# Kernel optimization log

Measured on AMD Instinct MI355X. Metric: run time of the kernel, lower is better.

## Reference

```python
import jax, jax.numpy as jnp
import numpy as np

N = 50000        # nodes
E = 800000       # edges (avg degree 16)
F_IN = 128
H = 128
C = 16


def setup_inputs() -> dict:
    key = jax.random.key(0)
    ks = jax.random.split(key, 12)
    x = jax.random.normal(ks[0], (N, F_IN), dtype=jnp.float32)
    edges = jax.random.randint(ks[1], (2, E), 0, N, dtype=jnp.int32)
    dims = [(F_IN, H), (H, H // 2), (H // 2, H // 4), (H // 4, H // 8), (H // 8, C)]
    params = {}
    for i, (di, do) in enumerate(dims):
        params[f"W{i+1}"] = jax.random.normal(ks[2 + 2 * i], (di, do), dtype=jnp.float32) * (1.0 / np.sqrt(di)).astype(np.float32)
        params[f"b{i+1}"] = jax.random.normal(ks[3 + 2 * i], (do,), dtype=jnp.float32) * 0.01
    return {"x": x, "edges": edges, **params}


def reference(x, edges, W1, b1, W2, b2, W3, b3, W4, b4, W5, b5):
    src, dst = edges[0], edges[1]
    ones = jnp.ones((E,), x.dtype)
    # symmetric ('both') normalization with degree clamped to >= 1 (DGL GraphConv default)
    out_deg = jnp.clip(jax.ops.segment_sum(ones, src, num_segments=N), 1.0, None)
    in_deg = jnp.clip(jax.ops.segment_sum(ones, dst, num_segments=N), 1.0, None)
    norm_src = (out_deg ** -0.5)[:, None]   # [N,1]
    norm_dst = (in_deg ** -0.5)[:, None]    # [N,1]

    def graph_conv(h, W, b):
        h = h @ W                                  # dense transform first (out <= in)
        msgs = (h * norm_src)[src]                 # [E, d_out] gather
        agg = jax.ops.segment_sum(msgs, dst, num_segments=N)  # scatter-add SpMM
        return agg * norm_dst + b

    h = x
    for W, b in ((W1, b1), (W2, b2), (W3, b3), (W4, b4), (W5, b5)):
        h = jax.nn.relu(graph_conv(h, W, b))
    return h
```

## Files before the change

kernel.cpp:

```cpp
#include <hip/hip_runtime.h>
#include <hip/hip_bf16.h>


#define THREADS 256
#define HIST_B 256
#define HWORDS 12500
#define RS_BLOCKS 196
#define G1BLKS 1564

typedef __attribute__((ext_vector_type(8))) short short8_t;
typedef __attribute__((ext_vector_type(4))) float float4_t;

__device__ __forceinline__ unsigned short f2bf_rne(float f) {
    unsigned u = __builtin_bit_cast(unsigned, f);
    unsigned r = u + 0x7fffu + ((u >> 16) & 1u);
    return (unsigned short)(r >> 16);
}
__device__ __forceinline__ float bf2f(unsigned short h) {
    return __builtin_bit_cast(float, ((unsigned)h) << 16);
}

template<int NT, bool NORM>
__device__ __forceinline__ void quant_epilogue(float4_t* acc, const float* __restrict__ norm,
                                               short* __restrict__ outq, float* __restrict__ qscale,
                                               int M, int blk, int tid,
                                               int ostride, int ocol0, int qstride, int qoff) {
    const int w    = tid >> 6;
    const int lane = tid & 63;
    const int ln   = lane & 15;
    const int quad = lane >> 4;
    const int orow = blk * 64 + w * 16 + quad * 4;
#pragma unroll
    for (int i = 0; i < 4; ++i) {
        int r = orow + i;
        float m = 0.f;
#pragma unroll
        for (int nt = 0; nt < NT; ++nt) m = fmaxf(m, fabsf(acc[nt][i]));
#pragma unroll
        for (int off = 1; off < 16; off <<= 1) m = fmaxf(m, __shfl_xor(m, off));
        float s = 1.f;
        if (NORM) s = (r < M) ? norm[r] : 0.f;
        float rowmax = m * s;
        float inv = (rowmax > 0.f) ? (32767.f / rowmax) : 0.f;
        if (r < M) {
            if (ln == 0) qscale[r * qstride + qoff] = rowmax * (1.f / 32767.f);
#pragma unroll
            for (int nt = 0; nt < NT; ++nt)
                outq[(size_t)r * ostride + ocol0 + nt * 16 + ln] =
                    (short)(int)__builtin_rintf(acc[nt][i] * s * inv);
        }
    }
}

template<int K, int NOUT, bool NORM>
__device__ __forceinline__ void gemm_core(const float* __restrict__ A,
                                          const short* lh, const short* ll,
                                          const float* __restrict__ norm,
                                          short* __restrict__ outq, float* __restrict__ qscale,
                                          int M, int blk, int tid,
                                          int ostride, int ocol0, int qstride, int qoff) {
    constexpr int Kp  = (K + 31) & ~31;
    constexpr int STR = Kp + 8;
    constexpr int NT  = NOUT / 16;
    const int w    = tid >> 6;
    const int lane = tid & 63;
    const int ln   = lane & 15;
    const int quad = lane >> 4;
    const int row  = blk * 64 + w * 16 + ln;
    const bool rv  = row < M;

    float4_t acc[NT];
#pragma unroll
    for (int i = 0; i < NT; ++i) acc[i] = (float4_t){0.f, 0.f, 0.f, 0.f};

#pragma unroll
    for (int kt = 0; kt < Kp / 32; ++kt) {
        const int k0 = kt * 32 + quad * 8;
        float a[8];
        if (rv && k0 < K) {
            float4 v0 = *(const float4*)&A[(size_t)row * K + k0];
            float4 v1 = *(const float4*)&A[(size_t)row * K + k0 + 4];
            a[0] = v0.x; a[1] = v0.y; a[2] = v0.z; a[3] = v0.w;
            a[4] = v1.x; a[5] = v1.y; a[6] = v1.z; a[7] = v1.w;
        } else {
#pragma unroll
            for (int j = 0; j < 8; ++j) a[j] = 0.f;
        }
        short8_t ahi, alo;
#pragma unroll
        for (int j = 0; j < 8; ++j) {
            unsigned short h = f2bf_rne(a[j]);
            ahi[j] = (short)h;
            alo[j] = (short)f2bf_rne(a[j] - bf2f(h));
        }
#pragma unroll
        for (int nt = 0; nt < NT; ++nt) {
            const int bidx = (nt * 16 + ln) * STR + kt * 32 + quad * 8;
            short8_t bh = *(const short8_t*)&lh[bidx];
            short8_t bl = *(const short8_t*)&ll[bidx];
            acc[nt] = __builtin_amdgcn_mfma_f32_16x16x32_bf16(ahi, bh, acc[nt], 0, 0, 0);
            acc[nt] = __builtin_amdgcn_mfma_f32_16x16x32_bf16(ahi, bl, acc[nt], 0, 0, 0);
            acc[nt] = __builtin_amdgcn_mfma_f32_16x16x32_bf16(alo, bh, acc[nt], 0, 0, 0);
        }
    }
    quant_epilogue<NT, NORM>(acc, norm, outq, qscale, M, blk, tid, ostride, ocol0, qstride, qoff);
}

template<int K, int NOUT, int DINP>
__device__ __forceinline__ void gemm_core_lds(const float* As,
                                              const short* lh, const short* ll,
                                              const float* __restrict__ norm,
                                              short* __restrict__ outq, float* __restrict__ qscale,
                                              int M, int blk, int tid) {
    constexpr int Kp  = (K + 31) & ~31;
    constexpr int STR = Kp + 8;
    constexpr int NT  = NOUT / 16;
    const int w    = tid >> 6;
    const int lane = tid & 63;
    const int ln   = lane & 15;
    const int quad = lane >> 4;
    const int rloc = w * 16 + ln;
    const bool rv  = (blk * 64 + rloc) < M;

    float4_t acc[NT];
#pragma unroll
    for (int i = 0; i < NT; ++i) acc[i] = (float4_t){0.f, 0.f, 0.f, 0.f};

#pragma unroll
    for (int kt = 0; kt < Kp / 32; ++kt) {
        const int k0 = kt * 32 + quad * 8;
        float a[8];
        if (rv && k0 < K) {
            float4 v0 = *(const float4*)&As[rloc * DINP + k0];
            float4 v1 = *(const float4*)&As[rloc * DINP + k0 + 4];
            a[0] = v0.x; a[1] = v0.y; a[2] = v0.z; a[3] = v0.w;
            a[4] = v1.x; a[5] = v1.y; a[6] = v1.z; a[7] = v1.w;
        } else {
#pragma unroll
            for (int j = 0; j < 8; ++j) a[j] = 0.f;
        }
        short8_t ahi, alo;
#pragma unroll
        for (int j = 0; j < 8; ++j) {
            unsigned short h = f2bf_rne(a[j]);
            ahi[j] = (short)h;
            alo[j] = (short)f2bf_rne(a[j] - bf2f(h));
        }
#pragma unroll
        for (int nt = 0; nt < NT; ++nt) {
            const int bidx = (nt * 16 + ln) * STR + kt * 32 + quad * 8;
            short8_t bh = *(const short8_t*)&lh[bidx];
            short8_t bl = *(const short8_t*)&ll[bidx];
            acc[nt] = __builtin_amdgcn_mfma_f32_16x16x32_bf16(ahi, bh, acc[nt], 0, 0, 0);
            acc[nt] = __builtin_amdgcn_mfma_f32_16x16x32_bf16(ahi, bl, acc[nt], 0, 0, 0);
            acc[nt] = __builtin_amdgcn_mfma_f32_16x16x32_bf16(alo, bh, acc[nt], 0, 0, 0);
        }
    }
    quant_epilogue<NT, true>(acc, norm, outq, qscale, M, blk, tid, NOUT, 0, 1, 0);
}

__device__ __forceinline__ void conv_one(const float* __restrict__ W, short* __restrict__ hi,
                                         short* __restrict__ lo, int K, int NOUT, int STR, int i) {
    int n = i / STR;
    int kk = i % STR;
    float v = (kk < K) ? W[(size_t)kk * NOUT + n] : 0.f;
    unsigned short h = f2bf_rne(v);
    hi[i] = (short)h;
    lo[i] = (short)f2bf_rne(v - bf2f(h));
}

__global__ __launch_bounds__(THREADS)
void packed0_kernel(const float* __restrict__ x, const float* __restrict__ W1,
                    const float* __restrict__ W2, const float* __restrict__ W3,
                    const float* __restrict__ W4, const float* __restrict__ W5,
                    short* __restrict__ tq, float* __restrict__ qscale2,
                    const int* __restrict__ src, const int* __restrict__ dst,
                    unsigned* __restrict__ p_src, unsigned* __restrict__ p_dst,
                    unsigned char* __restrict__ rank, int* __restrict__ flags,
                    short* w2h, short* w2l, short* w3h, short* w3l,
                    short* w4h, short* w4l, short* w5h, short* w5l,
                    int E, int chunk, int N) {
    __shared__ __align__(16) char smem[50048];
    const int blk = blockIdx.x;
    const int t = threadIdx.x;

    if (blk < G1BLKS) {
        const int h  = blk & 1;
        const int gb = blk >> 1;
        short* lh = (short*)smem;
        short* ll = (short*)smem + 8704;
        for (int j = t; j < 128 * 64; j += THREADS) {
            int kk = j >> 6, n = j & 63;
            float v = W1[kk * 128 + h * 64 + n];
            unsigned short hh = f2bf_rne(v);
            lh[n * 136 + kk] = (short)hh;
            ll[n * 136 + kk] = (short)f2bf_rne(v - bf2f(hh));
        }
        __syncthreads();
        gemm_core<128, 64, false>(x, lh, ll, nullptr, tq, qscale2, N, gb, t,
                                  128, h * 64, 2, h);
    } else if (blk < G1BLKS + 2 * HIST_B) {
        unsigned* bins = (unsigned*)smem;
        const int hb = blk - G1BLKS;
        const bool is_dst = hb < HIST_B;
        const int b = is_dst ? hb : hb - HIST_B;
        const int e0 = b * chunk;
        int e1 = e0 + chunk; if (e1 > E) e1 = E;
        const int* __restrict__ idx = is_dst ? dst : src;
        unsigned* __restrict__ pout = is_dst ? p_dst : p_src;

        for (int w = t; w < HWORDS; w += THREADS) bins[w] = 0;
        __syncthreads();
        for (int e = e0 + t; e < e1; e += THREADS) {
            int d = idx[e];
            unsigned sh = (unsigned)(d & 3) * 8u;
            unsigned old = atomicAdd(&bins[d >> 2], 1u << sh);
            if (is_dst) rank[e] = (unsigned char)((old >> sh) & 0xffu);
        }
        __syncthreads();
        for (int w = t; w < HWORDS; w += THREADS)
            pout[(size_t)b * HWORDS + w] = bins[w];
    } else {
        int cb = blk - G1BLKS - 2 * HIST_B;
        if (cb == 48) {
            flags[t] = 0;
            return;
        }
        int i = cb * THREADS + t;
        if (i < 8704)                        conv_one(W2, w2h, w2l, 128, 64, 136, i);
        else if ((i -= 8704) < 2304)         conv_one(W3, w3h, w3l, 64, 32, 72, i);
        else if ((i -= 2304) < 640)          conv_one(W4, w4h, w4l, 32, 16, 40, i);
        else { i -= 640;                     conv_one(W5, w5h, w5l, 16, 16, 40, i); }
    }
}

__global__ __launch_bounds__(THREADS)
void reduce_scan_kernel(const unsigned* __restrict__ p_src, unsigned* __restrict__ p_dst,
                        float* __restrict__ norm_src, float* __restrict__ norm_dst,
                        float* __restrict__ qscale2, int* __restrict__ row_ptr,
                        int* __restrict__ flags, int N) {
    __shared__ unsigned qd[4][64];
    __shared__ unsigned qs[4][64];
    __shared__ int sscan[64];
    __shared__ int bexcl_sh;
    const int t  = threadIdx.x;
    const int b  = blockIdx.x;
    const int q  = t >> 6;
    const int wl = t & 63;
    const int w  = b * 64 + wl;
    const bool wv = (w < HWORDS);

    unsigned vals[64];
    unsigned dsum = 0, ssum = 0;
    if (wv) {
#pragma unroll
        for (int i = 0; i < 64; ++i) {
            int c = q * 64 + i;
            vals[i] = p_dst[(size_t)c * HWORDS + w];
            dsum += vals[i];
        }
#pragma unroll
        for (int i = 0; i < 64; ++i) {
            int c = q * 64 + i;
            ssum += p_src[(size_t)c * HWORDS + w];
        }
    }
    qd[q][wl] = dsum;
    qs[q][wl] = ssum;
    __syncthreads();

    unsigned off = 0, dfull = 0, sfull = 0;
#pragma unroll
    for (int qq = 0; qq < 4; ++qq) {
        unsigned v = qd[qq][wl];
        if (qq < q) off += v;
        dfull += v;
        sfull += qs[qq][wl];
    }

    if (wv) {
        unsigned run = off;
#pragma unroll
        for (int i = 0; i < 64; ++i) {
            int c = q * 64 + i;
            p_dst[(size_t)c * HWORDS + w] = run;
            run += vals[i];
        }
    }

    int d0 = 0, d1 = 0, d2 = 0, d3 = 0, wdeg = 0;
    if (q == 0) {
        d0 = (int)(dfull & 0xffu); d1 = (int)((dfull >> 8) & 0xffu);
        d2 = (int)((dfull >> 16) & 0xffu); d3 = (int)(dfull >> 24);
        wdeg = d0 + d1 + d2 + d3;
        if (wv) {
#pragma unroll
            for (int l = 0; l < 4; ++l) {
                int node = 4 * w + l;
                int dd = (l == 0) ? d0 : (l == 1) ? d1 : (l == 2) ? d2 : d3;
                int ds = (int)((sfull >> (8 * l)) & 0xffu);
                norm_dst[node] = rsqrtf((float)(dd < 1 ? 1 : dd));
                float ns = rsqrtf((float)(ds < 1 ? 1 : ds));
                norm_src[node] = ns;
                qscale2[2 * node]     *= ns;
                qscale2[2 * node + 1] *= ns;
            }
        }
        sscan[wl] = wv ? wdeg : 0;
    }
    __syncthreads();
    for (int o = 1; o < 64; o <<= 1) {
        int u = 0;
        if (t < 64 && t >= o) u = sscan[t - o];
        __syncthreads();
        if (t < 64) sscan[t] += u;
        __syncthreads();
    }
    const int btotal = sscan[63];

    if (t == 0) atomicExch(&flags[b], btotal + 1);
    if (t < 64) {
        int v = 0;
        for (int p = t; p < b; p += 64) {
            int f;
            do { f = atomicAdd(&flags[p], 0); } while (f == 0);
            v += f - 1;
        }
#pragma unroll
        for (int o = 1; o < 64; o <<= 1) v += __shfl_xor(v, o);
        if (t == 0) bexcl_sh = v;
    }
    __syncthreads();

    if (q == 0 && wv) {
        int pre = bexcl_sh + sscan[wl] - wdeg;
        int n0 = 4 * w;
        row_ptr[n0 + 0] = pre; pre += d0;
        row_ptr[n0 + 1] = pre; pre += d1;
        row_ptr[n0 + 2] = pre; pre += d2;
        row_ptr[n0 + 3] = pre;
    }
    if (b == RS_BLOCKS - 1 && t == 0) row_ptr[N] = bexcl_sh + btotal;
}

__global__ __launch_bounds__(THREADS)
void scatter_kernel(const int* __restrict__ src, const int* __restrict__ dst,
                    const unsigned char* __restrict__ rank,
                    const int* __restrict__ row_ptr, const unsigned* __restrict__ p_dst,
                    int* __restrict__ col, int E, int chunk) {
    const int bc = blockIdx.x >> 1;
    const int hch = (chunk + 1) >> 1;
    const int e0 = bc * chunk;
    int e1 = e0 + chunk; if (e1 > E) e1 = E;
    int s = e0 + (blockIdx.x & 1) * hch;
    int send = s + hch; if (send > e1) send = e1;
    for (int e = s + threadIdx.x; e < send; e += THREADS) {
        int d = dst[e];
        unsigned sh = (unsigned)(d & 3) * 8u;
        unsigned pre = (p_dst[(size_t)bc * HWORDS + (d >> 2)] >> sh) & 0xffu;
        col[row_ptr[d] + (int)pre + (int)rank[e]] = src[e];
    }
}

template<int K, int NOUT>
__global__ __launch_bounds__(THREADS)
void gemm_mfma_kernel(const float* __restrict__ A, const short* __restrict__ wt_hi,
                      const short* __restrict__ wt_lo, const float* __restrict__ norm,
                      short* __restrict__ outq, float* __restrict__ qscale, int M) {
    constexpr int Kp  = (K + 31) & ~31;
    constexpr int STR = Kp + 8;

    __shared__ short lh[NOUT * STR];
    __shared__ short ll[NOUT * STR];

    const int tid = threadIdx.x;
    {
        constexpr int CNT = NOUT * STR / 2;
        const int* gh = (const int*)wt_hi;
        const int* gl = (const int*)wt_lo;
        int* sh = (int*)lh;
        int* sl = (int*)ll;
        for (int i = tid; i < CNT; i += THREADS) { sh[i] = gh[i]; sl[i] = gl[i]; }
    }
    __syncthreads();
    gemm_core<K, NOUT, true>(A, lh, ll, norm, outq, qscale, M, blockIdx.x, tid,
                             NOUT, 0, 1, 0);
}

template<int D, bool QS2>
__global__ __launch_bounds__(THREADS)
void agg_q_kernel(const short* __restrict__ tq, const float* __restrict__ qscale,
                  const int* __restrict__ row_ptr, const int* __restrict__ col,
                  const float* __restrict__ norm_dst, const float* __restrict__ bias,
                  float* __restrict__ out, int N) {
    constexpr int TPN = D / 8;
    constexpr int NPB = THREADS / TPN;
    const int tid  = threadIdx.x;
    const int ln   = tid % TPN;
    const int g    = tid / TPN;
    const int node = blockIdx.x * NPB + g;
    if (node >= N) return;

    const int half = QS2 ? (ln >> 3) : 0;
    const int beg = row_ptr[node];
    const int end = row_ptr[node + 1];

    float acc[8];
#pragma unroll
    for (int c = 0; c < 8; ++c) acc[c] = 0.f;

    auto scl = [&](int s) -> float {
        return QS2 ? qscale[2 * s + half] : qscale[s];
    };

    int j = beg;
    for (; j + 3 < end; j += 4) {
        int s0 = col[j], s1 = col[j + 1], s2 = col[j + 2], s3 = col[j + 3];
        short8_t v0 = *(const short8_t*)&tq[(size_t)s0 * D + ln * 8];
        short8_t v1 = *(const short8_t*)&tq[(size_t)s1 * D + ln * 8];
        short8_t v2 = *(const short8_t*)&tq[(size_t)s2 * D + ln * 8];
        short8_t v3 = *(const short8_t*)&tq[(size_t)s3 * D + ln * 8];
        float c0 = scl(s0), c1 = scl(s1), c2 = scl(s2), c3 = scl(s3);
#pragma unroll
        for (int c = 0; c < 8; ++c)
            acc[c] += (float)v0[c] * c0 + (float)v1[c] * c1
                    + (float)v2[c] * c2 + (float)v3[c] * c3;
    }
    for (; j < end; ++j) {
        int s0 = col[j];
        short8_t v0 = *(const short8_t*)&tq[(size_t)s0 * D + ln * 8];
        float c0 = scl(s0);
#pragma unroll
        for (int c = 0; c < 8; ++c) acc[c] += (float)v0[c] * c0;
    }

    float nd = norm_dst[node];
    float4 b0 = *(const float4*)&bias[ln * 8];
    float4 b1 = *(const float4*)&bias[ln * 8 + 4];
    float4 o0, o1;
    o0.x = fmaxf(acc[0] * nd + b0.x, 0.f);
    o0.y = fmaxf(acc[1] * nd + b0.y, 0.f);
    o0.z = fmaxf(acc[2] * nd + b0.z, 0.f);
    o0.w = fmaxf(acc[3] * nd + b0.w, 0.f);
    o1.x = fmaxf(acc[4] * nd + b1.x, 0.f);
    o1.y = fmaxf(acc[5] * nd + b1.y, 0.f);
    o1.z = fmaxf(acc[6] * nd + b1.z, 0.f);
    o1.w = fmaxf(acc[7] * nd + b1.w, 0.f);
    *(float4*)&out[(size_t)node * D + ln * 8] = o0;
    *(float4*)&out[(size_t)node * D + ln * 8 + 4] = o1;
}

template<int DIN, int NOUT>
__global__ __launch_bounds__(THREADS)
void fused_agg_gemm_kernel(const short* __restrict__ tq_in, const float* __restrict__ qs_in,
                           const int* __restrict__ row_ptr, const int* __restrict__ col,
                           const float* __restrict__ norm_dst, const float* __restrict__ bias,
                           const short* __restrict__ wt_hi, const short* __restrict__ wt_lo,
                           const float* __restrict__ norm_src,
                           short* __restrict__ tq_out, float* __restrict__ qs_out, int N) {
    constexpr int Kp   = (DIN + 31) & ~31;
    constexpr int STR  = Kp + 8;
    constexpr int DINP = DIN + 4;
    constexpr int TPN  = DIN / 8;

    __shared__ float As[64 * DINP];
    __shared__ short lh[NOUT * STR];
    __shared__ short ll[NOUT * STR];

    const int tid = threadIdx.x;
    {
        constexpr int CNT = NOUT * STR / 2;
        const int* gh = (const int*)wt_hi;
        const int* gl = (const int*)wt_lo;
        int* sh = (int*)lh;
        int* sl = (int*)ll;
        for (int i = tid; i < CNT; i += THREADS) { sh[i] = gh[i]; sl[i] = gl[i]; }
    }

    const int ln = tid % TPN;
    for (int n0 = tid / TPN; n0 < 64; n0 += THREADS / TPN) {
        const int node = blockIdx.x * 64 + n0;
        if (node < N) {
            const int beg = row_ptr[node];
            const int end = row_ptr[node + 1];
            float acc[8];
#pragma unroll
            for (int c = 0; c < 8; ++c) acc[c] = 0.f;
            int j = beg;
            for (; j + 3 < end; j += 4) {
                int s0 = col[j], s1 = col[j + 1], s2 = col[j + 2], s3 = col[j + 3];
                short8_t v0 = *(const short8_t*)&tq_in[(size_t)s0 * DIN + ln * 8];
                short8_t v1 = *(const short8_t*)&tq_in[(size_t)s1 * DIN + ln * 8];
                short8_t v2 = *(const short8_t*)&tq_in[(size_t)s2 * DIN + ln * 8];
                short8_t v3 = *(const short8_t*)&tq_in[(size_t)s3 * DIN + ln * 8];
                float c0 = qs_in[s0], c1 = qs_in[s1], c2 = qs_in[s2], c3 = qs_in[s3];
#pragma unroll
                for (int c = 0; c < 8; ++c)
                    acc[c] += (float)v0[c] * c0 + (float)v1[c] * c1
                            + (float)v2[c] * c2 + (float)v3[c] * c3;
            }
            for (; j < end; ++j) {
                int s0 = col[j];
                short8_t v0 = *(const short8_t*)&tq_in[(size_t)s0 * DIN + ln * 8];
                float c0 = qs_in[s0];
#pragma unroll
                for (int c = 0; c < 8; ++c) acc[c] += (float)v0[c] * c0;
            }
            float nd = norm_dst[node];
#pragma unroll
            for (int c = 0; c < 8; ++c)
                As[n0 * DINP + ln * 8 + c] = fmaxf(acc[c] * nd + bias[ln * 8 + c], 0.f);
        }
    }
    __syncthreads();

    gemm_core_lds<DIN, NOUT, DINP>(As, lh, ll, norm_src, tq_out, qs_out, N, blockIdx.x, tid);
}

extern "C" void kernel_launch(void* const* d_in, const int* in_sizes, int n_in,
                              void* d_out, int out_size, void* d_ws, size_t ws_size,
                              hipStream_t stream) {
    const float* x     = (const float*)d_in[0];
    const int*   edges = (const int*)d_in[1];
    const float* W1 = (const float*)d_in[2];  const float* b1 = (const float*)d_in[3];
    const float* W2 = (const float*)d_in[4];  const float* b2 = (const float*)d_in[5];
    const float* W3 = (const float*)d_in[6];  const float* b3 = (const float*)d_in[7];
    const float* W4 = (const float*)d_in[8];  const float* b4 = (const float*)d_in[9];
    const float* W5 = (const float*)d_in[10]; const float* b5 = (const float*)d_in[11];

    const int N = in_sizes[0] / 128;
    const int E = in_sizes[1] / 2;
    const int* src = edges;
    const int* dst = edges + E;

    char* ws = (char*)d_ws;
    size_t off = 0;
    auto carve = [&](size_t bytes) -> void* {
        void* p = ws + off;
        off += (bytes + 255) & ~(size_t)255;
        return p;
    };
    short* tqA      = (short*)carve((size_t)N * 128 * 2);
    short* tqB      = (short*)carve((size_t)N * 64 * 2);
    float* hbuf     = (float*)carve((size_t)N * 128 * 4);
    float* norm_src = (float*)carve((size_t)N * 4);
    float* norm_dst = (float*)carve((size_t)N * 4);
    int*   row_ptr  = (int*)carve((size_t)(N + 1) * 4);
    int*   col      = (int*)carve((size_t)E * 4);
    float* qsA      = (float*)carve((size_t)2 * N * 4);
    float* qsB      = (float*)carve((size_t)N * 4);
    int*   flags    = (int*)carve((size_t)256 * 4);
    short* wts      = (short*)carve((size_t)24576 * 2);
    unsigned* p_src = (unsigned*)carve((size_t)HIST_B * HWORDS * 4);
    unsigned* p_dst = (unsigned*)carve((size_t)HIST_B * HWORDS * 4);
    unsigned char* rank = (unsigned char*)carve((size_t)E);
    (void)ws_size;

    short* w2h = wts;            short* w2l = w2h + 8704;
    short* w3h = w2l + 8704;     short* w3l = w3h + 2304;
    short* w4h = w3l + 2304;     short* w4l = w4h + 640;
    short* w5h = w4l + 640;      short* w5l = w5h + 640;

    const int chunk = (E + HIST_B - 1) / HIST_B;
    const int gridG = (N + 63) / 64;

    packed0_kernel<<<G1BLKS + 2 * HIST_B + 49, THREADS, 0, stream>>>(
        x, W1, W2, W3, W4, W5, tqA, qsA, src, dst, p_src, p_dst, rank, flags,
        w2h, w2l, w3h, w3l, w4h, w4l, w5h, w5l, E, chunk, N);

    reduce_scan_kernel<<<RS_BLOCKS, THREADS, 0, stream>>>(
        p_src, p_dst, norm_src, norm_dst, qsA, row_ptr, flags, N);

    scatter_kernel<<<2 * HIST_B, THREADS, 0, stream>>>(src, dst, rank, row_ptr, p_dst, col, E, chunk);

    agg_q_kernel<128, true><<<(N + 15) / 16, THREADS, 0, stream>>>(
        tqA, qsA, row_ptr, col, norm_dst, b1, hbuf, N);

    gemm_mfma_kernel<128, 64><<<gridG, THREADS, 0, stream>>>(hbuf, w2h, w2l, norm_src, tqA, qsA, N);

    fused_agg_gemm_kernel<64, 32><<<gridG, THREADS, 0, stream>>>(
        tqA, qsA, row_ptr, col, norm_dst, b2, w3h, w3l, norm_src, tqB, qsB, N);
    fused_agg_gemm_kernel<32, 16><<<gridG, THREADS, 0, stream>>>(
        tqB, qsB, row_ptr, col, norm_dst, b3, w4h, w4l, norm_src, tqA, qsA, N);
    fused_agg_gemm_kernel<16, 16><<<gridG, THREADS, 0, stream>>>(
        tqA, qsA, row_ptr, col, norm_dst, b4, w5h, w5l, norm_src, tqB, qsB, N);

    agg_q_kernel<16, false><<<(N + 127) / 128, THREADS, 0, stream>>>(
        tqB, qsB, row_ptr, col, norm_dst, b5, (float*)d_out, N);
}
```

Before: 269.8 us.

## Quantize layer-1 aggregate to int16, split edge pairs, and halve histogram blocks

Layer-1 aggregation now writes an int16-quantized hidden state with a per-row scale instead of a float32 buffer, and the layer-2 GEMM reads that quantized input and folds the scale into its epilogue. This halves the intermediate write and read traffic. The new aggregation kernel splits each node's edges across two half-warps and combines them with a shuffle, giving more parallelism per node. The histogram block count is halved (HIST_B 256 to 128) and scatter now uses four sub-blocks per chunk, which changes work per block. The extra quantization step adds some precision loss.

```diff
diff --git a/kernel.cpp b/kernel.cpp
--- a/kernel.cpp
+++ b/kernel.cpp
@@ -3,10 +3,11 @@
 
 
 #define THREADS 256
-#define HIST_B 256
+#define HIST_B 128
 #define HWORDS 12500
 #define RS_BLOCKS 196
 #define G1BLKS 1564
+#define C4 (HIST_B / 4)
 
 typedef __attribute__((ext_vector_type(8))) short short8_t;
 typedef __attribute__((ext_vector_type(4))) float float4_t;
@@ -20,8 +21,9 @@
     return __builtin_bit_cast(float, ((unsigned)h) << 16);
 }
 
-template<int NT, bool NORM>
+template<int NT, bool NORM, bool ASCALE>
 __device__ __forceinline__ void quant_epilogue(float4_t* acc, const float* __restrict__ norm,
+                                               const float* __restrict__ ascale,
                                                short* __restrict__ outq, float* __restrict__ qscale,
                                                int M, int blk, int tid,
                                                int ostride, int ocol0, int qstride, int qoff) {
@@ -40,6 +42,7 @@
         for (int off = 1; off < 16; off <<= 1) m = fmaxf(m, __shfl_xor(m, off));
         float s = 1.f;
         if (NORM) s = (r < M) ? norm[r] : 0.f;
+        if (ASCALE && r < M) s *= ascale[r];
         float rowmax = m * s;
         float inv = (rowmax > 0.f) ? (32767.f / rowmax) : 0.f;
         if (r < M) {
@@ -103,7 +106,56 @@
             acc[nt] = __builtin_amdgcn_mfma_f32_16x16x32_bf16(alo, bh, acc[nt], 0, 0, 0);
         }
     }
-    quant_epilogue<NT, NORM>(acc, norm, outq, qscale, M, blk, tid, ostride, ocol0, qstride, qoff);
+    quant_epilogue<NT, NORM, false>(acc, norm, nullptr, outq, qscale, M, blk, tid,
+                                    ostride, ocol0, qstride, qoff);
+}
+
+template<int K, int NOUT>
+__device__ __forceinline__ void gemm_core_q(const short* __restrict__ Aq,
+                                            const float* __restrict__ ascale,
+                                            const short* lh, const short* ll,
+                                            const float* __restrict__ norm,
+                                            short* __restrict__ outq, float* __restrict__ qscale,
+                                            int M, int blk, int tid) {
+    constexpr int Kp  = (K + 31) & ~31;
+    constexpr int STR = Kp + 8;
+    constexpr int NT  = NOUT / 16;
+    const int w    = tid >> 6;
+    const int lane = tid & 63;
+    const int ln   = lane & 15;
+    const int quad = lane >> 4;
+    const int row  = blk * 64 + w * 16 + ln;
+    const bool rv  = row < M;
+
+    float4_t acc[NT];
+#pragma unroll
+    for (int i = 0; i < NT; ++i) acc[i] = (float4_t){0.f, 0.f, 0.f, 0.f};
+
+#pragma unroll
+    for (int kt = 0; kt < Kp / 32; ++kt) {
+        const int k0 = kt * 32 + quad * 8;
+        short8_t qv = (short8_t)(short)0;
+        if (rv && k0 < K) qv = *(const short8_t*)&Aq[(size_t)row * K + k0];
+        short8_t ahi, alo;
+#pragma unroll
+        for (int j = 0; j < 8; ++j) {
+            float a = (float)qv[j];
+            unsigned short h = f2bf_rne(a);
+            ahi[j] = (short)h;
+            alo[j] = (short)f2bf_rne(a - bf2f(h));
+        }
+#pragma unroll
+        for (int nt = 0; nt < NT; ++nt) {
+            const int bidx = (nt * 16 + ln) * STR + kt * 32 + quad * 8;
+            short8_t bh = *(const short8_t*)&lh[bidx];
+            short8_t bl = *(const short8_t*)&ll[bidx];
+            acc[nt] = __builtin_amdgcn_mfma_f32_16x16x32_bf16(ahi, bh, acc[nt], 0, 0, 0);
+            acc[nt] = __builtin_amdgcn_mfma_f32_16x16x32_bf16(ahi, bl, acc[nt], 0, 0, 0);
+            acc[nt] = __builtin_amdgcn_mfma_f32_16x16x32_bf16(alo, bh, acc[nt], 0, 0, 0);
+        }
+    }
+    quant_epilogue<NT, true, true>(acc, norm, ascale, outq, qscale, M, blk, tid,
+                                   NOUT, 0, 1, 0);
 }
 
 template<int K, int NOUT, int DINP>
@@ -156,7 +208,8 @@
             acc[nt] = __builtin_amdgcn_mfma_f32_16x16x32_bf16(alo, bh, acc[nt], 0, 0, 0);
         }
     }
-    quant_epilogue<NT, true>(acc, norm, outq, qscale, M, blk, tid, NOUT, 0, 1, 0);
+    quant_epilogue<NT, true, false>(acc, norm, nullptr, outq, qscale, M, blk, tid,
+                                    NOUT, 0, 1, 0);
 }
 
 __device__ __forceinline__ void conv_one(const float* __restrict__ W, short* __restrict__ hi,
@@ -250,18 +303,18 @@
     const int w  = b * 64 + wl;
     const bool wv = (w < HWORDS);
 
-    unsigned vals[64];
+    unsigned vals[C4];
     unsigned dsum = 0, ssum = 0;
     if (wv) {
 #pragma unroll
-        for (int i = 0; i < 64; ++i) {
-            int c = q * 64 + i;
+        for (int i = 0; i < C4; ++i) {
+            int c = q * C4 + i;
             vals[i] = p_dst[(size_t)c * HWORDS + w];
             dsum += vals[i];
         }
 #pragma unroll
-        for (int i = 0; i < 64; ++i) {
-            int c = q * 64 + i;
+        for (int i = 0; i < C4; ++i) {
+            int c = q * C4 + i;
             ssum += p_src[(size_t)c * HWORDS + w];
         }
     }
@@ -281,8 +334,8 @@
     if (wv) {
         unsigned run = off;
 #pragma unroll
-        for (int i = 0; i < 64; ++i) {
-            int c = q * 64 + i;
+        for (int i = 0; i < C4; ++i) {
+            int c = q * C4 + i;
             p_dst[(size_t)c * HWORDS + w] = run;
             run += vals[i];
         }
@@ -348,12 +401,13 @@
                     const unsigned char* __restrict__ rank,
                     const int* __restrict__ row_ptr, const unsigned* __restrict__ p_dst,
                     int* __restrict__ col, int E, int chunk) {
-    const int bc = blockIdx.x >> 1;
-    const int hch = (chunk + 1) >> 1;
+    const int bc  = blockIdx.x >> 2;
+    const int sub = blockIdx.x & 3;
+    const int qch = (chunk + 3) >> 2;
     const int e0 = bc * chunk;
     int e1 = e0 + chunk; if (e1 > E) e1 = E;
-    int s = e0 + (blockIdx.x & 1) * hch;
-    int send = s + hch; if (send > e1) send = e1;
+    int s = e0 + sub * qch;
+    int send = s + qch; if (send > e1) send = e1;
     for (int e = s + threadIdx.x; e < send; e += THREADS) {
         int d = dst[e];
         unsigned sh = (unsigned)(d & 3) * 8u;
@@ -362,11 +416,76 @@
     }
 }
 
+__global__ __launch_bounds__(THREADS)
+void agg1_q_kernel(const short* __restrict__ tq, const float* __restrict__ qscale2,
+                   const int* __restrict__ row_ptr, const int* __restrict__ col,
+                   const float* __restrict__ norm_dst, const float* __restrict__ bias,
+                   short* __restrict__ outq, float* __restrict__ qs_out, int N) {
+    const int tid  = threadIdx.x;
+    const int ln   = tid & 15;
+    const int ep   = (tid >> 4) & 1;
+    const int g    = tid >> 5;
+    const int node = blockIdx.x * 8 + g;
+    if (node >= N) return;
+
+    const int half = ln >> 3;
+    const int beg = row_ptr[node];
+    const int end = row_ptr[node + 1];
+
+    float acc[8];
+#pragma unroll
+    for (int c = 0; c < 8; ++c) acc[c] = 0.f;
+
+    int j = beg + ep;
+    for (; j + 2 < end; j += 4) {
+        int s0 = col[j];
+        int s1 = col[j + 2];
+        short8_t v0 = *(const short8_t*)&tq[(size_t)s0 * 128 + ln * 8];
+        short8_t v1 = *(const short8_t*)&tq[(size_t)s1 * 128 + ln * 8];
+        float c0 = qscale2[2 * s0 + half];
+        float c1 = qscale2[2 * s1 + half];
+#pragma unroll
+        for (int c = 0; c < 8; ++c)
+            acc[c] += (float)v0[c] * c0 + (float)v1[c] * c1;
+    }
+    if (j < end) {
+        int s0 = col[j];
+        short8_t v0 = *(const short8_t*)&tq[(size_t)s0 * 128 + ln * 8];
+        float c0 = qscale2[2 * s0 + half];
+#pragma unroll
+        for (int c = 0; c < 8; ++c) acc[c] += (float)v0[c] * c0;
+    }
+
+#pragma unroll
+    for (int c = 0; c < 8; ++c) acc[c] += __shfl_xor(acc[c], 16);
+
+    float nd = norm_dst[node];
+    float vals[8];
+    float m = 0.f;
+#pragma unroll
+    for (int c = 0; c < 8; ++c) {
+        vals[c] = fmaxf(acc[c] * nd + bias[ln * 8 + c], 0.f);
+        m = fmaxf(m, vals[c]);
+    }
+#pragma unroll
+    for (int off = 1; off < 16; off <<= 1) m = fmaxf(m, __shfl_xor(m, off));
+    float inv = (m > 0.f) ? (32767.f / m) : 0.f;
+
+    if (ep == 0) {
+        short8_t q;
+#pragma unroll
+        for (int c = 0; c < 8; ++c) q[c] = (short)(int)__builtin_rintf(vals[c] * inv);
+        *(short8_t*)&outq[(size_t)node * 128 + ln * 8] = q;
+        if (ln == 0) qs_out[node] = m * (1.f / 32767.f);
+    }
+}
+
 template<int K, int NOUT>
 __global__ __launch_bounds__(THREADS)
-void gemm_mfma_kernel(const float* __restrict__ A, const short* __restrict__ wt_hi,
-                      const short* __restrict__ wt_lo, const float* __restrict__ norm,
-                      short* __restrict__ outq, float* __restrict__ qscale, int M) {
+void gemm_mfma_q_kernel(const short* __restrict__ Aq, const float* __restrict__ ascale,
+                        const short* __restrict__ wt_hi, const short* __restrict__ wt_lo,
+                        const float* __restrict__ norm,
+                        short* __restrict__ outq, float* __restrict__ qscale, int M) {
     constexpr int Kp  = (K + 31) & ~31;
     constexpr int STR = Kp + 8;
 
@@ -383,11 +502,10 @@
         for (int i = tid; i < CNT; i += THREADS) { sh[i] = gh[i]; sl[i] = gl[i]; }
     }
     __syncthreads();
-    gemm_core<K, NOUT, true>(A, lh, ll, norm, outq, qscale, M, blockIdx.x, tid,
-                             NOUT, 0, 1, 0);
-}
-
-template<int D, bool QS2>
+    gemm_core_q<K, NOUT>(Aq, ascale, lh, ll, norm, outq, qscale, M, blockIdx.x, tid);
+}
+
+template<int D>
 __global__ __launch_bounds__(THREADS)
 void agg_q_kernel(const short* __restrict__ tq, const float* __restrict__ qscale,
                   const int* __restrict__ row_ptr, const int* __restrict__ col,
@@ -401,17 +519,12 @@
     const int node = blockIdx.x * NPB + g;
     if (node >= N) return;
 
-    const int half = QS2 ? (ln >> 3) : 0;
     const int beg = row_ptr[node];
     const int end = row_ptr[node + 1];
 
     float acc[8];
 #pragma unroll
     for (int c = 0; c < 8; ++c) acc[c] = 0.f;
-
-    auto scl = [&](int s) -> float {
-        return QS2 ? qscale[2 * s + half] : qscale[s];
-    };
 
     int j = beg;
     for (; j + 3 < end; j += 4) {
@@ -420,7 +533,7 @@
         short8_t v1 = *(const short8_t*)&tq[(size_t)s1 * D + ln * 8];
         short8_t v2 = *(const short8_t*)&tq[(size_t)s2 * D + ln * 8];
         short8_t v3 = *(const short8_t*)&tq[(size_t)s3 * D + ln * 8];
-        float c0 = scl(s0), c1 = scl(s1), c2 = scl(s2), c3 = scl(s3);
+        float c0 = qscale[s0], c1 = qscale[s1], c2 = qscale[s2], c3 = qscale[s3];
 #pragma unroll
         for (int c = 0; c < 8; ++c)
             acc[c] += (float)v0[c] * c0 + (float)v1[c] * c1
@@ -429,7 +542,7 @@
     for (; j < end; ++j) {
         int s0 = col[j];
         short8_t v0 = *(const short8_t*)&tq[(size_t)s0 * D + ln * 8];
-        float c0 = scl(s0);
+        float c0 = qscale[s0];
 #pragma unroll
         for (int c = 0; c < 8; ++c) acc[c] += (float)v0[c] * c0;
     }
@@ -542,13 +655,14 @@
     };
     short* tqA      = (short*)carve((size_t)N * 128 * 2);
     short* tqB      = (short*)carve((size_t)N * 64 * 2);
-    float* hbuf     = (float*)carve((size_t)N * 128 * 4);
+    short* tqH      = (short*)carve((size_t)N * 128 * 2);
     float* norm_src = (float*)carve((size_t)N * 4);
     float* norm_dst = (float*)carve((size_t)N * 4);
     int*   row_ptr  = (int*)carve((size_t)(N + 1) * 4);
     int*   col      = (int*)carve((size_t)E * 4);
     float* qsA      = (float*)carve((size_t)2 * N * 4);
     float* qsB      = (float*)carve((size_t)N * 4);
+    float* qsH      = (float*)carve((size_t)N * 4);
     int*   flags    = (int*)carve((size_t)256 * 4);
     short* wts      = (short*)carve((size_t)24576 * 2);
     unsigned* p_src = (unsigned*)carve((size_t)HIST_B * HWORDS * 4);
@@ -571,12 +685,13 @@
     reduce_scan_kernel<<<RS_BLOCKS, THREADS, 0, stream>>>(
         p_src, p_dst, norm_src, norm_dst, qsA, row_ptr, flags, N);
 
-    scatter_kernel<<<2 * HIST_B, THREADS, 0, stream>>>(src, dst, rank, row_ptr, p_dst, col, E, chunk);
-
-    agg_q_kernel<128, true><<<(N + 15) / 16, THREADS, 0, stream>>>(
-        tqA, qsA, row_ptr, col, norm_dst, b1, hbuf, N);
-
-    gemm_mfma_kernel<128, 64><<<gridG, THREADS, 0, stream>>>(hbuf, w2h, w2l, norm_src, tqA, qsA, N);
+    scatter_kernel<<<4 * HIST_B, THREADS, 0, stream>>>(src, dst, rank, row_ptr, p_dst, col, E, chunk);
+
+    agg1_q_kernel<<<(N + 7) / 8, THREADS, 0, stream>>>(
+        tqA, qsA, row_ptr, col, norm_dst, b1, tqH, qsH, N);
+
+    gemm_mfma_q_kernel<128, 64><<<gridG, THREADS, 0, stream>>>(
+        tqH, qsH, w2h, w2l, norm_src, tqA, qsA, N);
 
     fused_agg_gemm_kernel<64, 32><<<gridG, THREADS, 0, stream>>>(
         tqA, qsA, row_ptr, col, norm_dst, b2, w3h, w3l, norm_src, tqB, qsB, N);
@@ -585,6 +700,6 @@
     fused_agg_gemm_kernel<16, 16><<<gridG, THREADS, 0, stream>>>(
         tqA, qsA, row_ptr, col, norm_dst, b4, w5h, w5l, norm_src, tqB, qsB, N);
 
-    agg_q_kernel<16, false><<<(N + 127) / 128, THREADS, 0, stream>>>(
+    agg_q_kernel<16><<<(N + 127) / 128, THREADS, 0, stream>>>(
         tqB, qsB, row_ptr, col, norm_dst, b5, (float*)d_out, N);
 }
```

Result: faster. 260.7 us (-3.4%).
